# Kernel tuning notes

Measured on AMD Instinct MI355X. Metric: run time of the kernel, lower is better.

## Reference

```python
import jax, jax.numpy as jnp
from jax import lax
import numpy as np

D_MODEL = 768
D_STATE = 64
D_CONV = 4
EXPAND = 2
D_INNER = EXPAND * D_MODEL          # 1536
HEADDIM = 64
H = D_INNER // HEADDIM              # 24 heads
CONV_DIM = D_INNER + 2 * D_STATE    # 1664 (x, B, C share the conv)
D_IN_PROJ = 2 * D_INNER + 2 * D_STATE + H  # z, xBC, dt
BATCH, SEQ = 4, 4096


def _mamba2(x, in_w, conv_w, conv_b, dt_bias, A_log, Dp, norm_w, out_w):
    """Mamba2 forward (ngroups=1, no in/out-proj bias), faithful to mamba_ssm reference path."""
    Bb, L, _ = x.shape
    zxbcdt = x @ in_w.T                                   # (B,L,D_IN_PROJ)
    z = zxbcdt[..., :D_INNER]
    xBC = zxbcdt[..., D_INNER:D_INNER + CONV_DIM]
    dt = zxbcdt[..., D_INNER + CONV_DIM:]                 # (B,L,H)
    # causal depthwise conv1d over time + SiLU
    xBC = xBC.transpose(0, 2, 1)                          # (B,C,L)
    xBC = lax.conv_general_dilated(xBC, conv_w, (1,), [(D_CONV - 1, 0)],
                                   feature_group_count=CONV_DIM,
                                   dimension_numbers=('NCH', 'OIH', 'NCH'))
    xBC = jax.nn.silu(xBC + conv_b[None, :, None]).transpose(0, 2, 1)
    xs = xBC[..., :D_INNER].reshape(Bb, L, H, HEADDIM)    # (B,L,H,P)
    Bc = xBC[..., D_INNER:D_INNER + D_STATE]              # (B,L,N)
    Cc = xBC[..., D_INNER + D_STATE:]                     # (B,L,N)
    dt = jax.nn.softplus(dt + dt_bias)                    # (B,L,H)
    dA = jnp.exp(dt * (-jnp.exp(A_log)))                  # (B,L,H)
    dtx = dt[..., None] * xs                              # (B,L,H,P)

    def step(h, inp):
        dA_t, dtx_t, B_t, C_t = inp
        h = h * dA_t[:, :, None, None] + jnp.einsum('bhp,bn->bhpn', dtx_t, B_t)
        y = jnp.einsum('bhpn,bn->bhp', h, C_t)
        return h, y

    h0 = jnp.zeros((Bb, H, HEADDIM, D_STATE), x.dtype)
    _, ys = lax.scan(step, h0, (jnp.moveaxis(dA, 1, 0), jnp.moveaxis(dtx, 1, 0),
                                jnp.moveaxis(Bc, 1, 0), jnp.moveaxis(Cc, 1, 0)))
    y = jnp.moveaxis(ys, 0, 1) + Dp[None, None, :, None] * xs  # skip term D*x
    y = y.reshape(Bb, L, D_INNER)
    # RMSNormGated (norm_before_gate=False): gate then normalize
    y = y * jax.nn.silu(z)
    y = y * lax.rsqrt(jnp.mean(y * y, -1, keepdims=True) + 1e-5) * norm_w
    return y @ out_w.T                                    # (B,L,D_MODEL)


def _mamba_params(key, scale=0.02):
    ks = jax.random.split(key, 5)
    in_w = jax.random.normal(ks[0], (D_IN_PROJ, D_MODEL), jnp.float32) * scale
    conv_w = jax.random.normal(ks[1], (CONV_DIM, 1, D_CONV), jnp.float32) * 0.2
    conv_b = jnp.zeros((CONV_DIM,), jnp.float32)
    dt = jax.random.uniform(ks[2], (H,), jnp.float32, 0.001, 0.1)
    dt_bias = dt + jnp.log(-jnp.expm1(-dt))               # inverse softplus
    A_log = jnp.log(jax.random.uniform(ks[3], (H,), jnp.float32, 1.0, 16.0))
    Dp = jnp.ones((H,), jnp.float32)
    norm_w = jnp.ones((D_INNER,), jnp.float32)
    out_w = jax.random.normal(ks[4], (D_MODEL, D_INNER), jnp.float32) * scale
    return in_w, conv_w, conv_b, dt_bias, A_log, Dp, norm_w, out_w


def setup_inputs() -> dict:
    key = jax.random.key(0)
    kx, kf, kb, kw = jax.random.split(key, 4)
    x = jax.random.normal(kx, (BATCH, SEQ, D_MODEL), jnp.float32)
    f = _mamba_params(kf)
    b = _mamba_params(kb)
    fus_w = jax.random.normal(kw, (D_MODEL, 2 * D_MODEL), jnp.float32) * 0.02
    fus_b = jnp.zeros((D_MODEL,), jnp.float32)
    names = ['in_w', 'conv_w', 'conv_b', 'dt_bias', 'A_log', 'D', 'norm_w', 'out_w']
    inp = {'x': x, 'fus_w': fus_w, 'fus_b': fus_b}
    for n, v in zip(names, f):
        inp['f_' + n] = v
    for n, v in zip(names, b):
        inp['b_' + n] = v
    return inp


def reference(x, fus_w, fus_b,
              f_in_w, f_conv_w, f_conv_b, f_dt_bias, f_A_log, f_D, f_norm_w, f_out_w,
              b_in_w, b_conv_w, b_conv_b, b_dt_bias, b_A_log, b_D, b_norm_w, b_out_w):
    out_f = _mamba2(x, f_in_w, f_conv_w, f_conv_b, f_dt_bias, f_A_log, f_D, f_norm_w, f_out_w)
    out_b = jnp.flip(_mamba2(jnp.flip(x, 1), b_in_w, b_conv_w, b_conv_b,
                             b_dt_bias, b_A_log, b_D, b_norm_w, b_out_w), 1)
    out = jnp.concatenate([out_f, out_b], axis=-1)        # (B,L,2*D_MODEL)
    return out @ fus_w.T + fus_b
```

## Files before the change

### kernel.cpp

```cpp
#include <hip/hip_runtime.h>
#include <hip/hip_bf16.h>


#define BATCHN 4
#define SEQL 4096
#define DMODEL 768
#define DINNER 1536
#define DSTATE 64
#define HN 24
#define CONVDIM 1664
#define NROWS_XBC 3200
#define NTOK (BATCHN*SEQL)
#define NCHUNK 64
#define LS 72
#define GBUF (128 * 32)

typedef short v8s __attribute__((ext_vector_type(8)));
typedef unsigned short v8u __attribute__((ext_vector_type(8)));
typedef float v4f __attribute__((ext_vector_type(4)));
typedef unsigned int v2u32 __attribute__((ext_vector_type(2)));
typedef __hip_bfloat16 bf16;

__device__ __forceinline__ int flip_row(int r) {
  return (r & ~4095) | (4095 - (r & 4095));
}
__device__ __forceinline__ float us2f(unsigned short u) {
  return __uint_as_float(((unsigned int)u) << 16);
}
__device__ __forceinline__ unsigned short f2us(float f) {
  bf16 b = __float2bfloat16(f);
  return __builtin_bit_cast(unsigned short, b);
}
__device__ __forceinline__ void async16(const unsigned short* g, unsigned short* l) {
  __builtin_amdgcn_global_load_lds(
      (const __attribute__((address_space(1))) unsigned int*)(const void*)g,
      (__attribute__((address_space(3))) unsigned int*)(void*)l, 16, 0, 0);
}


__global__ void cast_x_kernel(const float* __restrict__ x, bf16* __restrict__ xf) {
  int idx = blockIdx.x * 256 + threadIdx.x;
  v4f v = *(const v4f*)(x + (size_t)idx * 4);
  v2u32 o;
  o[0] = (unsigned int)f2us(v[0]) | ((unsigned int)f2us(v[1]) << 16);
  o[1] = (unsigned int)f2us(v[2]) | ((unsigned int)f2us(v[3]) << 16);
  *(v2u32*)((unsigned short*)xf + (size_t)idx * 4) = o;
}

__global__ void cast_kernel(const float* __restrict__ src, bf16* __restrict__ dst) {
  int idx = blockIdx.x * 256 + threadIdx.x;
  v4f v = *(const v4f*)(src + (size_t)idx * 4);
  v2u32 o;
  o[0] = (unsigned int)f2us(v[0]) | ((unsigned int)f2us(v[1]) << 16);
  o[1] = (unsigned int)f2us(v[2]) | ((unsigned int)f2us(v[3]) << 16);
  *(v2u32*)((unsigned short*)dst + (size_t)idx * 4) = o;
}

__global__ void cast_strided_kernel(const float* __restrict__ src, bf16* __restrict__ dst,
                                    int cols, int src_stride) {
  int idx4 = (blockIdx.x * 256 + threadIdx.x) * 4;
  int j = idx4 / cols, m = idx4 % cols;
  v4f v = *(const v4f*)(src + (size_t)j * src_stride + m);
  v2u32 o;
  o[0] = (unsigned int)f2us(v[0]) | ((unsigned int)f2us(v[1]) << 16);
  o[1] = (unsigned int)f2us(v[2]) | ((unsigned int)f2us(v[3]) << 16);
  *(v2u32*)((unsigned short*)dst + idx4) = o;
}

__global__ void transpose_ow_kernel(const float* __restrict__ src, bf16* __restrict__ dst) {
  int idx4 = (blockIdx.x * 256 + threadIdx.x) * 4;
  int k = idx4 / DMODEL, c0 = idx4 % DMODEL;
  unsigned short u[4];
#pragma unroll
  for (int i = 0; i < 4; i++)
    u[i] = f2us(src[(size_t)(c0 + i) * DINNER + k]);
  v2u32 o;
  o[0] = (unsigned int)u[0] | ((unsigned int)u[1] << 16);
  o[1] = (unsigned int)u[2] | ((unsigned int)u[3] << 16);
  *(v2u32*)((unsigned short*)dst + idx4) = o;
}

template <bool OUT_BF16>
__global__ __launch_bounds__(256) void gemm_lds(
    const bf16* __restrict__ A, const bf16* __restrict__ B, void* __restrict__ C,
    int K, int ldc, int flip_a, int flip_c, int accum, const float* __restrict__ bias) {
  __shared__ unsigned short sA[2 * GBUF];
  __shared__ unsigned short sB[2 * GBUF];
  int tid = threadIdx.x;
  int wave = tid >> 6, lane = tid & 63;
  int l15 = lane & 15, quad = lane >> 4;
  int m0 = blockIdx.x * 128, n0 = blockIdx.y * 128;
  int mw = (wave >> 1) * 64, nw = (wave & 1) * 64;

  int srow = wave * 32 + (lane >> 2);
  int scol = (lane & 3) * 8;
  const unsigned short* Ap = (const unsigned short*)A;
  const unsigned short* Bp = (const unsigned short*)B;
  int ar0 = m0 + srow, ar1 = m0 + srow + 16;
  if (flip_a) { ar0 = flip_row(ar0); ar1 = flip_row(ar1); }
  const unsigned short* ga0 = Ap + (size_t)ar0 * K + scol;
  const unsigned short* ga1 = Ap + (size_t)ar1 * K + scol;
  const unsigned short* gb0 = Bp + (size_t)(n0 + srow) * K + scol;
  const unsigned short* gb1 = Bp + (size_t)(n0 + srow + 16) * K + scol;
  int lo0 = (wave * 32) * 32;
  int lo1 = (wave * 32 + 16) * 32;

  v4f acc[4][4];
#pragma unroll
  for (int i = 0; i < 4; i++)
#pragma unroll
    for (int j = 0; j < 4; j++) acc[i][j] = {0.f, 0.f, 0.f, 0.f};

  async16(ga0, &sA[lo0]);
  async16(ga1, &sA[lo1]);
  async16(gb0, &sB[lo0]);
  async16(gb1, &sB[lo1]);
  __syncthreads();

  int nt = K >> 5;
  for (int t = 0; t < nt; t++) {
    int cur = (t & 1) * GBUF;
    if (t + 1 < nt) {
      int k0 = (t + 1) << 5;
      int nx = ((t + 1) & 1) * GBUF;
      async16(ga0 + k0, &sA[nx + lo0]);
      async16(ga1 + k0, &sA[nx + lo1]);
      async16(gb0 + k0, &sB[nx + lo0]);
      async16(gb1 + k0, &sB[nx + lo1]);
    }
    v8s af[4], bfr[4];
#pragma unroll
    for (int i = 0; i < 4; i++)
      af[i] = *(const v8s*)&sA[cur + (mw + i * 16 + l15) * 32 + quad * 8];
#pragma unroll
    for (int j = 0; j < 4; j++)
      bfr[j] = *(const v8s*)&sB[cur + (nw + j * 16 + l15) * 32 + quad * 8];
#pragma unroll
    for (int i = 0; i < 4; i++)
#pragma unroll
      for (int j = 0; j < 4; j++)
        acc[i][j] = __builtin_amdgcn_mfma_f32_16x16x32_bf16(af[i], bfr[j], acc[i][j], 0, 0, 0);
    __syncthreads();
  }

  float bv[4];
#pragma unroll
  for (int j = 0; j < 4; j++) bv[j] = bias ? bias[n0 + nw + j * 16 + l15] : 0.f;

#pragma unroll
  for (int i = 0; i < 4; i++) {
#pragma unroll
    for (int r2 = 0; r2 < 4; r2++) {
      int row = m0 + mw + i * 16 + quad * 4 + r2;
      int orow = flip_c ? flip_row(row) : row;
#pragma unroll
      for (int j = 0; j < 4; j++) {
        int col = n0 + nw + j * 16 + l15;
        float v = acc[i][j][r2] + bv[j];
        size_t off = (size_t)orow * ldc + col;
        if (OUT_BF16) {
          ((bf16*)C)[off] = __float2bfloat16(v);
        } else {
          float* Cf = (float*)C;
          if (accum) v += Cf[off];
          Cf[off] = v;
        }
      }
    }
  }
}

__global__ __launch_bounds__(256) void dt_fused_kernel(
    const float* __restrict__ x,
    const float* __restrict__ in_w0, const float* __restrict__ in_w1,
    const float* __restrict__ dt_bias0, const float* __restrict__ dt_bias1,
    const float* __restrict__ A_log0, const float* __restrict__ A_log1,
    float* __restrict__ dt0, float* __restrict__ dl0,
    float* __restrict__ dt1, float* __restrict__ dl1) {
  __shared__ float sXT[64][128];
  __shared__ float sW[24][64];
  int tid = threadIdx.x;
  int tok2 = tid & 63, cg = tid >> 6;
  int dir = blockIdx.y;
  int tok_base = blockIdx.x * 128;

  int st_tok = tid >> 1, st_k0 = (tid & 1) * 32;
  const float* xg = x + (size_t)(tok_base + st_tok) * DMODEL + st_k0;
  const float* wb = dir ? in_w1 : in_w0;
  const float* wrow = wb + (size_t)NROWS_XBC * DMODEL;

  float acc0[6], acc1[6];
#pragma unroll
  for (int c = 0; c < 6; c++) { acc0[c] = 0.f; acc1[c] = 0.f; }

#pragma unroll 1
  for (int kc = 0; kc < 12; kc++) {
#pragma unroll
    for (int i = 0; i < 8; i++) {
      v4f v = *(const v4f*)(xg + kc * 64 + i * 4);
#pragma unroll
      for (int j = 0; j < 4; j++) sXT[st_k0 + i * 4 + j][st_tok] = v[j];
    }
    for (int i = tid; i < 24 * 16; i += 256) {
      int col = i >> 4, k4 = i & 15;
      *(v4f*)&sW[col][k4 * 4] =
          *(const v4f*)(wrow + (size_t)col * DMODEL + kc * 64 + k4 * 4);
    }
    __syncthreads();
#pragma unroll 2
    for (int k4 = 0; k4 < 16; k4++) {
      float xa[4], xb[4];
#pragma unroll
      for (int j = 0; j < 4; j++) {
        xa[j] = sXT[k4 * 4 + j][tok2];
        xb[j] = sXT[k4 * 4 + j][tok2 + 64];
      }
#pragma unroll
      for (int c = 0; c < 6; c++) {
        v4f wv = *(const v4f*)&sW[cg * 6 + c][k4 * 4];
#pragma unroll
        for (int j = 0; j < 4; j++) {
          acc0[c] = fmaf(xa[j], wv[j], acc0[c]);
          acc1[c] = fmaf(xb[j], wv[j], acc1[c]);
        }
      }
    }
    __syncthreads();
  }

  const float* dtB = dir ? dt_bias1 : dt_bias0;
  const float* Alg = dir ? A_log1 : A_log0;
  float* dto = dir ? dt1 : dt0;
  float* dlo = dir ? dl1 : dl0;
#pragma unroll
  for (int t = 0; t < 2; t++) {
    int r = tok_base + t * 64 + tok2;
    size_t row = dir ? (size_t)flip_row(r) : (size_t)r;
#pragma unroll
    for (int c = 0; c < 6; c++) {
      int h = cg * 6 + c;
      float v = (t ? acc1[c] : acc0[c]) + dtB[h];
      float dtv = (v > 20.f) ? v : log1pf(expf(v));
      dto[row * HN + h] = dtv;
      dlo[row * HN + h] = -dtv * expf(Alg[h]);
    }
  }
}

__global__ void conv_bc_kernel(const bf16* __restrict__ xbcr,
                               const float* __restrict__ conv_w,
                               const float* __restrict__ conv_b,
                               bf16* __restrict__ Bblob, bf16* __restrict__ Cblob) {
  int idx = blockIdx.x * 256 + threadIdx.x;
  int token = idx >> 4, oct = idx & 15;
  int b = token >> 12, l = token & 4095, c = l >> 6, s = l & 63;
  int ch0 = 1536 + oct * 8;
  const unsigned short* xp = (const unsigned short*)xbcr;
  v8u tv[4];
#pragma unroll
  for (int j = 0; j < 4; j++) {
    int ls = l - 3 + j;
    v8u z = {0, 0, 0, 0, 0, 0, 0, 0};
    tv[j] = z;
    if (ls >= 0)
      tv[j] = *(const v8u*)(xp + (size_t)((b << 12) | ls) * CONVDIM + ch0);
  }
  v8u ov;
#pragma unroll
  for (int e = 0; e < 8; e++) {
    int ch = ch0 + e;
    const float* w4 = conv_w + ch * 4;
    float acc = conv_b[ch];
#pragma unroll
    for (int j = 0; j < 4; j++) acc += us2f(tv[j][e]) * w4[j];
    ov[e] = f2us(acc / (1.f + __expf(-acc)));
  }
  size_t base = ((size_t)((b * 64 + c) * 64 + s)) * 64;
  int ch7 = oct * 8;
  if (ch7 < 64) *(v8u*)((unsigned short*)Bblob + base + ch7) = ov;
  else          *(v8u*)((unsigned short*)Cblob + base + ch7 - 64) = ov;
}

__global__ __launch_bounds__(256) void chunk_intra_kernel(
    const bf16* __restrict__ xbcr, const bf16* __restrict__ Bblob,
    const bf16* __restrict__ Cblob, const float* __restrict__ conv_w,
    const float* __restrict__ conv_b, const float* __restrict__ dtb,
    const float* __restrict__ dlb, const float* __restrict__ Dp,
    bf16* __restrict__ Yblob, bf16* __restrict__ Gblob, float* __restrict__ laq) {
  int blk = blockIdx.x;
  int c = blk & 63, bh = blk >> 6;
  int h = bh % HN, b = bh / HN;
  int tid = threadIdx.x, lane = tid & 63, wv = tid >> 6;
  int l15 = lane & 15, quad = lane >> 4;
  int tok0 = b * SEQL + c * 64;

  __shared__ unsigned short sXT[64][LS];
  __shared__ unsigned short sB [64][LS];
  __shared__ unsigned short sBT[64][LS];
  __shared__ unsigned short sC [64][LS];
  __shared__ union { unsigned short rawX[67][72]; unsigned short W[64][LS]; } sU;
  __shared__ float sla[64], sdt[64], sdG[64];

  for (int i = tid; i < 536; i += 256) {
    int r = i >> 3, j = i & 7;
    int l = c * 64 + r - 3;
    v8u v = {0, 0, 0, 0, 0, 0, 0, 0};
    if (l >= 0)
      v = *(const v8u*)((const unsigned short*)xbcr +
                        (size_t)(b * SEQL + l) * CONVDIM + h * 64 + j * 8);
    *(v8u*)&sU.rawX[r][j * 8] = v;
  }
  {
    const v8u* gB = (const v8u*)((const unsigned short*)Bblob + ((size_t)(b * 64 + c)) * 4096);
    const v8u* gC = (const v8u*)((const unsigned short*)Cblob + ((size_t)(b * 64 + c)) * 4096);
    int r0 = tid >> 3, g0 = tid & 7;
#pragma unroll
    for (int it = 0; it < 2; it++) {
      int row = r0 + it * 32;
      *(v8u*)&sB[row][g0 * 8] = gB[row * 8 + g0];
      *(v8u*)&sC[row][g0 * 8] = gC[row * 8 + g0];
    }
  }
  if (wv == 0) {
    float dtv = dtb[(size_t)(tok0 + lane) * HN + h];
    float lg = dlb[(size_t)(tok0 + lane) * HN + h];
#pragma unroll
    for (int d = 1; d < 64; d <<= 1) {
      float o = __shfl_up(lg, d);
      if (lane >= d) lg += o;
    }
    sla[lane] = lg;
    sdt[lane] = dtv;
    float la63 = __shfl(lg, 63);
    sdG[lane] = __expf(la63 - lg) * dtv;
    if (lane == 63) laq[blk] = __expf(la63);
  }
  __syncthreads();

  float Dh = Dp[h];
  {
    int s = lane;
#pragma unroll
    for (int o = 0; o < 2; o++) {
      int p0 = (wv * 2 + o) * 8;
      v8u r0 = *(const v8u*)&sU.rawX[s + 0][p0];
      v8u r1 = *(const v8u*)&sU.rawX[s + 1][p0];
      v8u r2 = *(const v8u*)&sU.rawX[s + 2][p0];
      v8u r3 = *(const v8u*)&sU.rawX[s + 3][p0];
#pragma unroll
      for (int pp = 0; pp < 8; pp++) {
        int ch = h * 64 + p0 + pp;
        const float* w4 = conv_w + ch * 4;
        float acc = conv_b[ch] + us2f(r0[pp]) * w4[0] + us2f(r1[pp]) * w4[1] +
                    us2f(r2[pp]) * w4[2] + us2f(r3[pp]) * w4[3];
        sXT[p0 + pp][s] = f2us(acc / (1.f + __expf(-acc)));
      }
    }
#pragma unroll
    for (int it = 0; it < 16; it++) {
      int n = wv + it * 4;
      sBT[n][s] = f2us(us2f(sB[s][n]) * sdG[s]);
    }
  }
  __syncthreads();

  {
    v4f acc[4];
#pragma unroll
    for (int j = 0; j < 4; j++) acc[j] = {0.f, 0.f, 0.f, 0.f};
    __builtin_amdgcn_s_setprio(1);
#pragma unroll
    for (int k0 = 0; k0 < 2; k0++) {
      v8s a = *(const v8s*)&sC[16 * wv + l15][k0 * 32 + quad * 8];
#pragma unroll
      for (int j = 0; j < 4; j++) {
        v8s bb = *(const v8s*)&sB[16 * j + l15][k0 * 32 + quad * 8];
        acc[j] = __builtin_amdgcn_mfma_f32_16x16x32_bf16(a, bb, acc[j], 0, 0, 0);
      }
    }
    __builtin_amdgcn_s_setprio(0);
    float lat[4];
#pragma unroll
    for (int r = 0; r < 4; r++) lat[r] = sla[16 * wv + quad * 4 + r];
#pragma unroll
    for (int j = 0; j < 4; j++) {
      int s = 16 * j + l15;
      float las = sla[s], dts = sdt[s];
#pragma unroll
      for (int r = 0; r < 4; r++) {
        int t = 16 * wv + quad * 4 + r;
        float w = (s <= t) ? __expf(lat[r] - las) * dts * acc[j][r] : 0.f;
        sU.W[t][s] = f2us(w);
      }
    }
  }
  __syncthreads();

  {
    v4f ya[4], ga[4];
#pragma unroll
    for (int j = 0; j < 4; j++) {
      ya[j] = {0.f, 0.f, 0.f, 0.f};
      ga[j] = {0.f, 0.f, 0.f, 0.f};
    }
    __builtin_amdgcn_s_setprio(1);
#pragma unroll
    for (int k0 = 0; k0 < 2; k0++) {
      v8s aw = *(const v8s*)&sU.W[16 * wv + l15][k0 * 32 + quad * 8];
      v8s ax = *(const v8s*)&sXT[16 * wv + l15][k0 * 32 + quad * 8];
#pragma unroll
      for (int j = 0; j < 4; j++) {
        v8s bx = *(const v8s*)&sXT[16 * j + l15][k0 * 32 + quad * 8];
        v8s bt = *(const v8s*)&sBT[16 * j + l15][k0 * 32 + quad * 8];
        ya[j] = __builtin_amdgcn_mfma_f32_16x16x32_bf16(aw, bx, ya[j], 0, 0, 0);
        ga[j] = __builtin_amdgcn_mfma_f32_16x16x32_bf16(ax, bt, ga[j], 0, 0, 0);
      }
    }
    __builtin_amdgcn_s_setprio(0);
#pragma unroll
    for (int j = 0; j < 4; j++) {
      int col = 16 * j + l15;
#pragma unroll
      for (int r = 0; r < 4; r++) {
        int row = 16 * wv + quad * 4 + r;
        float yv = ya[j][r] + Dh * us2f(sXT[col][row]);
        sB[row][col] = f2us(yv);
        sC[row][col] = f2us(ga[j][r]);
      }
    }
  }
  __syncthreads();

  {
    v8u* gY = (v8u*)(Yblob + (size_t)blk * 4096);
    v8u* gG = (v8u*)(Gblob + (size_t)blk * 4096);
#pragma unroll
    for (int it = 0; it < 2; it++) {
      int i = tid + it * 256;
      int row = i >> 3, j = i & 7;
      gY[row * 8 + j] = *(const v8u*)&sB[row][j * 8];
      gG[row * 8 + j] = *(const v8u*)&sC[row][j * 8];
    }
  }
}

__global__ __launch_bounds__(256) void state_scan_kernel(
    bf16* __restrict__ blob, const float* __restrict__ laq) {
  int bh = blockIdx.x;
  int tid = threadIdx.x;
  size_t base = (size_t)bh * 64 * 4096 + (size_t)(tid >> 2) * 64 + (size_t)(tid & 3) * 16;
  float S[16];
#pragma unroll
  for (int i = 0; i < 16; i++) S[i] = 0.f;
  for (int c = 0; c < 64; c++) {
    float q = laq[bh * 64 + c];
    unsigned short* gp = (unsigned short*)blob + base + (size_t)c * 4096;
    v8u ga = ((v8u*)gp)[0], gb = ((v8u*)gp)[1];
    v8u pa, pb;
#pragma unroll
    for (int i = 0; i < 8; i++) {
      pa[i] = f2us(S[i]);
      pb[i] = f2us(S[8 + i]);
    }
    ((v8u*)gp)[0] = pa;
    ((v8u*)gp)[1] = pb;
#pragma unroll
    for (int i = 0; i < 8; i++) {
      S[i] = q * S[i] + us2f(ga[i]);
      S[8 + i] = q * S[8 + i] + us2f(gb[i]);
    }
  }
}

__global__ __launch_bounds__(256) void chunk_inter_kernel(
    const bf16* __restrict__ Cblob, const float* __restrict__ dlb,
    const bf16* __restrict__ blob, bf16* __restrict__ Yblob) {
  int blk = blockIdx.x;
  int c = blk & 63, bh = blk >> 6;
  int h = bh % HN, b = bh / HN;
  int tid = threadIdx.x, lane = tid & 63, wv = tid >> 6;
  int l15 = lane & 15, quad = lane >> 4;
  int tok0 = b * SEQL + c * 64;

  __shared__ unsigned short sC[64][LS];
  __shared__ unsigned short sY[64][LS];
  __shared__ float sel[64];

  {
    const v8u* gC = (const v8u*)((const unsigned short*)Cblob + ((size_t)(b * 64 + c)) * 4096);
    int r0 = tid >> 3, g0 = tid & 7;
#pragma unroll
    for (int it = 0; it < 2; it++) {
      int row = r0 + it * 32;
      *(v8u*)&sC[row][g0 * 8] = gC[row * 8 + g0];
    }
  }
  if (wv == 0) {
    float lg = dlb[(size_t)(tok0 + lane) * HN + h];
#pragma unroll
    for (int d = 1; d < 64; d <<= 1) {
      float o = __shfl_up(lg, d);
      if (lane >= d) lg += o;
    }
    sel[lane] = __expf(lg);
  }
  __syncthreads();
  {
    v4f acc[4];
#pragma unroll
    for (int j = 0; j < 4; j++) acc[j] = {0.f, 0.f, 0.f, 0.f};
    const unsigned short* gS = (const unsigned short*)blob + (size_t)blk * 4096;
    __builtin_amdgcn_s_setprio(1);
#pragma unroll
    for (int k0 = 0; k0 < 2; k0++) {
      v8s a = *(const v8s*)&sC[16 * wv + l15][k0 * 32 + quad * 8];
#pragma unroll
      for (int j = 0; j < 4; j++) {
        v8s bS = *(const v8s*)(gS + (size_t)(16 * j + l15) * 64 + k0 * 32 + quad * 8);
        acc[j] = __builtin_amdgcn_mfma_f32_16x16x32_bf16(a, bS, acc[j], 0, 0, 0);
      }
    }
    __builtin_amdgcn_s_setprio(0);
    float selt[4];
#pragma unroll
    for (int r = 0; r < 4; r++) selt[r] = sel[16 * wv + quad * 4 + r];
#pragma unroll
    for (int j = 0; j < 4; j++)
#pragma unroll
      for (int r = 0; r < 4; r++)
        sY[16 * wv + quad * 4 + r][16 * j + l15] = f2us(selt[r] * acc[j][r]);
  }
  __syncthreads();
  {
    v8u* gY = (v8u*)(Yblob + (size_t)blk * 4096);
#pragma unroll
    for (int it = 0; it < 2; it++) {
      int i = tid + it * 256;
      int row = i >> 3, j = i & 7;
      v8u old = gY[row * 8 + j];
      v8u add = *(const v8u*)&sY[row][j * 8];
      v8u outv;
#pragma unroll
      for (int e = 0; e < 8; e++) outv[e] = f2us(us2f(old[e]) + us2f(add[e]));
      gY[row * 8 + j] = outv;
    }
  }
}

__global__ __launch_bounds__(256) void norm_kernel(
    const bf16* __restrict__ Yblob, const bf16* __restrict__ z,
    const float* __restrict__ norm_w, bf16* __restrict__ out) {
  int token = blockIdx.x;
  int tid = threadIdx.x;
  int b = token >> 12, l = token & 4095, c = l >> 6, t = l & 63;
  const unsigned short* zp = (const unsigned short*)z + (size_t)token * DINNER;
  float vals[6];
  float ss = 0.f;
#pragma unroll
  for (int i = 0; i < 3; i++) {
    int q = tid + i * 256;
    int ch = q * 2;
    int hh = ch >> 6, p = ch & 63;
    size_t yi = ((((size_t)(b * HN + hh)) * 64 + c) * 64 + t) * 64 + p;
    unsigned int yv2 = *(const unsigned int*)((const unsigned short*)Yblob + yi);
    unsigned int zv2 = *(const unsigned int*)(zp + ch);
#pragma unroll
    for (int e = 0; e < 2; e++) {
      float yv = us2f((unsigned short)((yv2 >> (16 * e)) & 0xffff));
      float zv = us2f((unsigned short)((zv2 >> (16 * e)) & 0xffff));
      float g = zv / (1.f + __expf(-zv));
      float v = yv * g;
      vals[i * 2 + e] = v;
      ss += v * v;
    }
  }
  for (int off = 32; off > 0; off >>= 1) ss += __shfl_down(ss, off);
  __shared__ float sred[4];
  if ((tid & 63) == 0) sred[tid >> 6] = ss;
  __syncthreads();
  float tot = sred[0] + sred[1] + sred[2] + sred[3];
  float scale = rsqrtf(tot / (float)DINNER + 1e-5f);
#pragma unroll
  for (int i = 0; i < 3; i++) {
    int q = tid + i * 256;
    int ch = q * 2;
    unsigned int o =
        (unsigned int)f2us(vals[i * 2] * scale * norm_w[ch]) |
        ((unsigned int)f2us(vals[i * 2 + 1] * scale * norm_w[ch + 1]) << 16);
    *(unsigned int*)((unsigned short*)out + (size_t)token * DINNER + ch) = o;
  }
}

extern "C" void kernel_launch(void* const* d_in, const int* in_sizes, int n_in,
                              void* d_out, int out_size, void* d_ws, size_t ws_size,
                              hipStream_t stream) {
  const float* x = (const float*)d_in[0];
  const float* fus_w = (const float*)d_in[1];
  const float* fus_b = (const float*)d_in[2];
  const float* in_w[2] = {(const float*)d_in[3], (const float*)d_in[11]};
  const float* conv_w[2] = {(const float*)d_in[4], (const float*)d_in[12]};
  const float* conv_b[2] = {(const float*)d_in[5], (const float*)d_in[13]};
  const float* dt_bias[2] = {(const float*)d_in[6], (const float*)d_in[14]};
  const float* A_log[2] = {(const float*)d_in[7], (const float*)d_in[15]};
  const float* Dp[2] = {(const float*)d_in[8], (const float*)d_in[16]};
  const float* norm_w[2] = {(const float*)d_in[9], (const float*)d_in[17]};
  const float* out_w[2] = {(const float*)d_in[10], (const float*)d_in[18]};
  (void)in_sizes; (void)n_in;

  char* ws = (char*)d_ws;
  size_t off = 0;
  auto alloc = [&](size_t bytes) {
    size_t o = off;
    off = (off + bytes + 255) & ~(size_t)255;
    return o;
  };
  bf16* x_bf  = (bf16*)(ws + alloc((size_t)NTOK * DMODEL * 2));
  bf16* w_in  = (bf16*)(ws + alloc((size_t)NROWS_XBC * DMODEL * 2));
  bf16* wf1   = (bf16*)(ws + alloc((size_t)DMODEL * DMODEL * 2));
  bf16* owT   = (bf16*)(ws + alloc((size_t)DINNER * DMODEL * 2));
  bf16* wc    = (bf16*)(ws + alloc((size_t)DMODEL * DINNER * 2));
  bf16* xbcr  = (bf16*)(ws + alloc((size_t)NTOK * CONVDIM * 2));
  float* dtb0 = (float*)(ws + alloc((size_t)NTOK * HN * 4));
  float* dlb0 = (float*)(ws + alloc((size_t)NTOK * HN * 4));
  float* dtb1 = (float*)(ws + alloc((size_t)NTOK * HN * 4));
  float* dlb1 = (float*)(ws + alloc((size_t)NTOK * HN * 4));
  float* laq  = (float*)(ws + alloc((size_t)BATCHN * HN * NCHUNK * 4));
  bf16* Bblob = (bf16*)(ws + alloc((size_t)NTOK * DSTATE * 2));
  bf16* Cblob = (bf16*)(ws + alloc((size_t)NTOK * DSTATE * 2));
  bf16* Gblob = (bf16*)(ws + alloc((size_t)NTOK * DINNER * 2));
  bf16* Yblob = (bf16*)(ws + alloc((size_t)NTOK * DINNER * 2));
  bf16* zbuf  = Gblob;
  bf16* ynorm = xbcr;
  float* dtbs[2] = {dtb0, dtb1};
  float* dlbs[2] = {dlb0, dlb1};

  if (ws_size < off) {
    hipMemsetAsync(d_out, 0, (size_t)out_size * 4, stream);
    return;
  }

  cast_x_kernel<<<(NTOK * DMODEL) / 1024, 256, 0, stream>>>(x, x_bf);
  dt_fused_kernel<<<dim3(NTOK / 128, 2), 256, 0, stream>>>(
      x, in_w[0], in_w[1], dt_bias[0], dt_bias[1], A_log[0], A_log[1],
      dtb0, dlb0, dtb1, dlb1);

  for (int dir = 0; dir < 2; dir++) {
    cast_kernel<<<(NROWS_XBC * DMODEL) / 1024, 256, 0, stream>>>(in_w[dir], w_in);
    gemm_lds<true><<<dim3(NTOK / 128, CONVDIM / 128), 256, 0, stream>>>(
        x_bf, w_in + (size_t)DINNER * DMODEL, xbcr, DMODEL, CONVDIM, dir, 0, 0, nullptr);
    conv_bc_kernel<<<(NTOK * 16) / 256, 256, 0, stream>>>(
        xbcr, conv_w[dir], conv_b[dir], Bblob, Cblob);
    chunk_intra_kernel<<<BATCHN * HN * NCHUNK, 256, 0, stream>>>(
        xbcr, Bblob, Cblob, conv_w[dir], conv_b[dir], dtbs[dir], dlbs[dir], Dp[dir],
        Yblob, Gblob, laq);
    state_scan_kernel<<<BATCHN * HN, 256, 0, stream>>>(Gblob, laq);
    chunk_inter_kernel<<<BATCHN * HN * NCHUNK, 256, 0, stream>>>(Cblob, dlbs[dir], Gblob, Yblob);
    gemm_lds<true><<<dim3(NTOK / 128, DINNER / 128), 256, 0, stream>>>(
        x_bf, w_in, zbuf, DMODEL, DINNER, dir, 0, 0, nullptr);
    norm_kernel<<<NTOK, 256, 0, stream>>>(Yblob, zbuf, norm_w[dir], ynorm);
    cast_strided_kernel<<<(DMODEL * DMODEL) / 1024, 256, 0, stream>>>(
        fus_w + dir * DMODEL, wf1, DMODEL, 2 * DMODEL);
    transpose_ow_kernel<<<(DINNER * DMODEL) / 1024, 256, 0, stream>>>(out_w[dir], owT);
    gemm_lds<true><<<dim3(DMODEL / 128, DINNER / 128), 256, 0, stream>>>(
        wf1, owT, wc, DMODEL, DINNER, 0, 0, 0, nullptr);
    gemm_lds<false><<<dim3(NTOK / 128, DMODEL / 128), 256, 0, stream>>>(
        ynorm, wc, d_out, DINNER, DMODEL, 0, dir, dir, dir == 0 ? fus_b : nullptr);
  }
}
```

Measured before the change: 918.3 us.

## Triple-buffer GEMM LDS tiles with prefetch distance two and explicit vmcnt waits

The bf16 MFMA GEMM moves from double-buffered to triple-buffered LDS staging and issues async global-to-LDS loads two K-tiles ahead. Each iteration waits with s_waitcnt vmcnt(4) plus a single barrier, replacing the full __syncthreads at the end of each iteration. The aim is to hide global load latency and cut one barrier per K step. The cost is higher LDS use per block (48KB instead of 32KB), which may lower occupancy. The bias load is also hoisted ahead of the main loop.

```diff
diff --git a/kernel.cpp b/kernel.cpp
--- a/kernel.cpp
+++ b/kernel.cpp
@@ -84,13 +84,17 @@
 __global__ __launch_bounds__(256) void gemm_lds(
     const bf16* __restrict__ A, const bf16* __restrict__ B, void* __restrict__ C,
     int K, int ldc, int flip_a, int flip_c, int accum, const float* __restrict__ bias) {
-  __shared__ unsigned short sA[2 * GBUF];
-  __shared__ unsigned short sB[2 * GBUF];
+  __shared__ unsigned short sA[3 * GBUF];
+  __shared__ unsigned short sB[3 * GBUF];
   int tid = threadIdx.x;
   int wave = tid >> 6, lane = tid & 63;
   int l15 = lane & 15, quad = lane >> 4;
   int m0 = blockIdx.x * 128, n0 = blockIdx.y * 128;
   int mw = (wave >> 1) * 64, nw = (wave & 1) * 64;
+
+  float bv[4];
+#pragma unroll
+  for (int j = 0; j < 4; j++) bv[j] = bias ? bias[n0 + nw + j * 16 + l15] : 0.f;
 
   int srow = wave * 32 + (lane >> 2);
   int scol = (lane & 3) * 8;
@@ -111,23 +115,29 @@
 #pragma unroll
     for (int j = 0; j < 4; j++) acc[i][j] = {0.f, 0.f, 0.f, 0.f};
 
-  async16(ga0, &sA[lo0]);
-  async16(ga1, &sA[lo1]);
-  async16(gb0, &sB[lo0]);
-  async16(gb1, &sB[lo1]);
-  __syncthreads();
+  auto stage = [&](int t, int bo) {
+    int k0 = t << 5;
+    async16(ga0 + k0, &sA[bo + lo0]);
+    async16(ga1 + k0, &sA[bo + lo1]);
+    async16(gb0 + k0, &sB[bo + lo0]);
+    async16(gb1 + k0, &sB[bo + lo1]);
+  };
 
   int nt = K >> 5;
+  stage(0, 0);
+  stage(1, GBUF);
+  int cur = 0, stg = 2 * GBUF;
+
+#pragma unroll 1
   for (int t = 0; t < nt; t++) {
-    int cur = (t & 1) * GBUF;
     if (t + 1 < nt) {
-      int k0 = (t + 1) << 5;
-      int nx = ((t + 1) & 1) * GBUF;
-      async16(ga0 + k0, &sA[nx + lo0]);
-      async16(ga1 + k0, &sA[nx + lo1]);
-      async16(gb0 + k0, &sB[nx + lo0]);
-      async16(gb1 + k0, &sB[nx + lo1]);
-    }
+      asm volatile("s_waitcnt vmcnt(4)" ::: "memory");
+    } else {
+      asm volatile("s_waitcnt vmcnt(0)" ::: "memory");
+    }
+    __builtin_amdgcn_s_barrier();
+    __builtin_amdgcn_sched_barrier(0);
+    if (t + 2 < nt) stage(t + 2, stg);
     v8s af[4], bfr[4];
 #pragma unroll
     for (int i = 0; i < 4; i++)
@@ -140,12 +150,9 @@
 #pragma unroll
       for (int j = 0; j < 4; j++)
         acc[i][j] = __builtin_amdgcn_mfma_f32_16x16x32_bf16(af[i], bfr[j], acc[i][j], 0, 0, 0);
-    __syncthreads();
-  }
-
-  float bv[4];
-#pragma unroll
-  for (int j = 0; j < 4; j++) bv[j] = bias ? bias[n0 + nw + j * 16 + l15] : 0.f;
+    cur = (cur == 2 * GBUF) ? 0 : cur + GBUF;
+    stg = (stg == 2 * GBUF) ? 0 : stg + GBUF;
+  }
 
 #pragma unroll
   for (int i = 0; i < 4; i++) {
```

Measured after the change: 921.4 us. About the same (+0.3%).
